# Kernel optimization log

Hardware: AMD Instinct MI355X
Metric: run time of the kernel (lower is better)

The kernel has to match this reference:

```python
import jax, jax.numpy as jnp
import numpy as np

B, F, L = 16384, 32, 64
FEAT, DOM, R = 100000, 8, 16
D_IN = F * L  # 2048
N_HIDDEN = 3  # hidden_units = [256, 128, 1]


def _p(k, shape, scale=0.05):
    return jax.random.normal(k, shape, dtype=jnp.float32) * scale


def setup_inputs() -> dict:
    key = jax.random.key(0)
    ks = jax.random.split(key, 32)
    return {
        'x': jax.random.randint(ks[0], (B, F), 0, FEAT),
        'd': jax.random.randint(ks[1], (B,), 0, DOM),
        'emb': _p(ks[2], (FEAT, L)),
        # share MLP: 2048 -> 1024 -> 512 (ReLU after each)
        'sW0': _p(ks[3], (D_IN, 1024)), 'sb0': _p(ks[4], (1024,)),
        'sW1': _p(ks[5], (1024, 512)), 'sb1': _p(ks[6], (512,)),
        # domain layer: 512 -> 256 shared kernel + per-domain LoRA
        'Dk0': _p(ks[7], (512, 256)), 'Db0': _p(ks[8], (256,)),
        'DA0': _p(ks[9], (DOM, 512, R)), 'DB0': _p(ks[10], (DOM, R, 256)), 'Dlb0': _p(ks[11], (DOM, 256)),
        # task layers: 256 -> 128 -> 1 shared kernels + per-task LoRA
        'Tk0': _p(ks[12], (256, 128)), 'Tb0': _p(ks[13], (128,)),
        'Tk1': _p(ks[14], (128, 1)), 'Tb1': _p(ks[15], (1,)),
        'TA0': _p(ks[16], (2, 256, R)), 'TB0': _p(ks[17], (2, R, 128)), 'Tlb0': _p(ks[18], (2, 128)),
        'TA1': _p(ks[19], (2, 128, R)), 'TB1': _p(ks[20], (2, R, 1)), 'Tlb1': _p(ks[21], (2, 1)),
        # gate hypernet + heads
        'gW0': _p(ks[22], (D_IN, 1024)), 'gb0': _p(ks[23], (1024,)),
        'gW1': _p(ks[24], (1024, 512)), 'gb1': _p(ks[25], (512,)),
        'h0W': _p(ks[26], (512, 4)), 'h0b': _p(ks[27], (4,)),
        'h1W': _p(ks[28], (512, 4)), 'h1b': _p(ks[29], (4,)),
    }


def _mlp2(x, W0, b0, W1, b1):
    return jax.nn.relu(jax.nn.relu(x @ W0 + b0) @ W1 + b1)


def _forward(x, d, emb, sW0, sb0, sW1, sb1, Dk0, Db0, DA0, DB0, Dlb0,
             Tk0, Tb0, Tk1, Tb1, TA0, TB0, Tlb0, TA1, TB1, Tlb1,
             gW0, gb0, gW1, gb1, h0W, h0b, h1W, h1b):
    x_emb = emb[x].reshape(x.shape[0], -1)          # (B, dnn_dim)
    x_dnn = _mlp2(x_emb, sW0, sb0, sW1, sb1)        # (B, 512)

    # ---- domain layer (i=0), k=0 -> ReLU applied ----
    share = x_dnn @ Dk0 + Db0                        # (B, 256)
    lora = jnp.einsum('bi,bir->br', x_dnn, DA0[d])   # per-sample domain LoRA gather+matmul
    lora = jnp.einsum('br,bro->bo', lora, DB0[d]) + Dlb0[d]
    d_dnn = jax.nn.relu(share + lora)                # activated
    # d_share / d_lora kept PRE-activation, as in source

    t_dnn = [d_dnn, d_dnn]
    t_share = [share, share]
    t_lora = [lora, lora]
    t_sl, t_ls = [], []
    Tk, Tb = [Tk0, Tk1], [Tb0, Tb1]
    TA, TB, Tlb = [TA0, TA1], [TB0, TB1], [Tlb0, Tlb1]

    k = 1  # shared counter, faithfully incremented per (i, t) step
    for i in range(2):
        for t in range(2):
            ds = t_dnn[t] @ Tk[i] + Tb[i]
            ss = t_share[t] @ Tk[i] + Tb[i]
            ls = t_lora[t] @ Tk[i] + Tb[i]
            t_ls.append(ls)
            A, Bm, lb = TA[i][t], TB[i][t], Tlb[i][t]
            dl = (t_dnn[t] @ A) @ Bm + lb[None, :]
            sl = (t_share[t] @ A) @ Bm + lb[None, :]
            ll = (t_lora[t] @ A) @ Bm + lb[None, :]
            t_dnn[t] = ds + dl
            t_share[t] = ss
            t_lora[t] = ll
            t_sl.append(sl)
            if k + 1 < N_HIDDEN:  # only fires at (i=0, t=0)
                t_dnn[t] = jax.nn.relu(t_dnn[t])
                t_share[t] = jax.nn.relu(t_share[t])
                t_lora[t] = jax.nn.relu(t_lora[t])
                t_sl[t] = jax.nn.relu(t_sl[t])
                t_ls[t] = jax.nn.relu(t_ls[t])
                k += 1

    # ---- gating (hypernet sees detached embedding) ----
    hyper = _mlp2(jax.lax.stop_gradient(x_emb), gW0, gb0, gW1, gb1)
    gates = [jax.nn.sigmoid(hyper @ h0W + h0b), jax.nn.sigmoid(hyper @ h1W + h1b)]

    outs = []
    for t in range(2):
        g = gates[t]
        # t_dnn/t_share/t_lora are (B,1); t_sl[t]/t_ls[t] are (B,128) from i=0 -> broadcast (B,128)
        outs.append(t_dnn[t] - g[:, 0:1] * t_share[t] - g[:, 1:2] * t_lora[t]
                    - g[:, 2:3] * t_sl[t] - g[:, 3:4] * t_ls[t])
    return jnp.stack(outs)  # (2, B, 128)


def reference(x, d, emb, sW0, sb0, sW1, sb1, Dk0, Db0, DA0, DB0, Dlb0,
              Tk0, Tb0, Tk1, Tb1, TA0, TB0, Tlb0, TA1, TB1, Tlb1,
              gW0, gb0, gW1, gb1, h0W, h0b, h1W, h1b):
    return _forward(x, d, emb, sW0, sb0, sW1, sb1, Dk0, Db0, DA0, DB0, Dlb0,
                    Tk0, Tb0, Tk1, Tb1, TA0, TB0, Tlb0, TA1, TB1, Tlb1,
                    gW0, gb0, gW1, gb1, h0W, h0b, h1W, h1b)
```

## Files before the change

kernel.cpp:

```cpp
#include <hip/hip_runtime.h>
#include <hip/hip_bf16.h>

#define BATCH 16384

typedef __attribute__((ext_vector_type(4))) float f32x4;
typedef __attribute__((ext_vector_type(8))) short bf16x8;

__device__ inline float b2f(unsigned short u) {
    union { unsigned u; float f; } c; c.u = ((unsigned)u) << 16; return c.f;
}
__device__ inline unsigned short f2b(float f) {
    __hip_bfloat16 h = __float2bfloat16(f);
    return *(unsigned short*)&h;
}

#define GLL16(g, l)                                                            \
    __builtin_amdgcn_global_load_lds(                                          \
        (const __attribute__((address_space(1))) void*)(g),                    \
        (__attribute__((address_space(3))) void*)(l), 16, 0, 0)

__global__ __launch_bounds__(256) void k_prep(
    const float* __restrict__ sW0, const float* __restrict__ gW0,
    const float* __restrict__ sW1, const float* __restrict__ gW1,
    const float* __restrict__ Dk0, const float* __restrict__ Tk0,
    const float* __restrict__ TA0,
    const float* __restrict__ sb0, const float* __restrict__ gb0,
    const float* __restrict__ sb1, const float* __restrict__ gb1,
    const float* __restrict__ Tb0, const float* __restrict__ DA0,
    const float* __restrict__ DB0, const float* __restrict__ emb,
    unsigned short* __restrict__ W1t, unsigned short* __restrict__ W2cat,
    unsigned short* __restrict__ Dk0t, unsigned short* __restrict__ Tcat,
    float* __restrict__ b1cat, float* __restrict__ b2cat, float* __restrict__ tb0c,
    unsigned short* __restrict__ DA0b, unsigned short* __restrict__ DB0b,
    unsigned short* __restrict__ embB)
{
    int id = blockIdx.x;
    const int tid = threadIdx.x;
    __shared__ float t[32][33];
    auto tcvt = [&](const float* src, int K, int N, unsigned short* dst,
                    int dst_off, int dst_ld, int bx, int by) {
        int k0 = by * 32, n0 = bx * 32;
        int tx = tid & 31, ty = tid >> 5;
        #pragma unroll
        for (int s = 0; s < 32; s += 8) {
            int k = k0 + ty + s, n = n0 + tx;
            t[ty + s][tx] = (k < K && n < N) ? src[(size_t)k * N + n] : 0.f;
        }
        __syncthreads();
        #pragma unroll
        for (int s = 0; s < 32; s += 8) {
            int n = n0 + ty + s, k = k0 + tx;
            if (n < N && k < K)
                dst[(size_t)(dst_off + n) * dst_ld + k] = f2b(t[tx][ty + s]);
        }
    };
    if (id < 4096) { int z = id >> 11, rem = id & 2047;
        tcvt(z ? gW0 : sW0, 2048, 1024, W1t, z * 1024, 2048, rem & 31, rem >> 5); return; }
    id -= 4096;
    if (id < 1024) { int z = id >> 9, rem = id & 511;
        tcvt(z ? gW1 : sW1, 1024, 512, W2cat, z * 512, 1024, rem & 15, rem >> 4); return; }
    id -= 1024;
    if (id < 128) { tcvt(Dk0, 512, 256, Dk0t, 0, 512, id & 7, id >> 3); return; }
    id -= 128;
    if (id < 32)  { tcvt(Tk0, 256, 128, Tcat, 0, 256, id & 3, id >> 2); return; }
    id -= 32;
    if (id < 16)  { int z = id >> 3;
        tcvt(TA0 + z * 256 * 16, 256, 16, Tcat, 128 + z * 16, 256, 0, id & 7); return; }
    id -= 16;
    if (id < 397) {
        int i = id * 256 + tid;
        if (i < 1024)            { b1cat[i] = sb0[i]; return; }
        if (i < 2048)            { b1cat[i] = gb0[i - 1024]; return; }
        if (i < 2560)            { b2cat[i - 2048] = sb1[i - 2048]; return; }
        if (i < 3072)            { b2cat[i - 2560 + 512] = gb1[i - 2560]; return; }
        if (i < 3200)            { tb0c[i - 3072] = Tb0[i - 3072]; return; }
        if (i < 3232)            { tb0c[i - 3200 + 128] = 0.f; return; }
        i -= 3232;
        if (i < 65536)           { DA0b[i] = f2b(DA0[i]); return; }
        i -= 65536;
        if (i < 32768)           { DB0b[i] = f2b(DB0[i]); return; }
        return;
    }
    id -= 397;
    {
        int e = (id * 256 + tid) * 4;
        if (e < 100000 * 64) {
            float4 v = *(const float4*)(emb + e);
            ushort4 o = { f2b(v.x), f2b(v.y), f2b(v.z), f2b(v.w) };
            *(ushort4*)(embB + e) = o;
        }
    }
}

template<int RELU, int OUTBF16, int GATHER>
__global__ __launch_bounds__(512, 2) void k_gemm256(
    const unsigned short* __restrict__ A, int lda, long Az,
    const unsigned short* __restrict__ Bt, int K, long Bz,
    const float* __restrict__ bias, int biasz,
    void* __restrict__ C, int ldc, long Cz,
    int N, const int* __restrict__ xsrc, const unsigned short* __restrict__ embB)
{
    extern __shared__ char smem_raw[];
    const int NT = K >> 6;
    const int tid  = threadIdx.x;
    const int lane = tid & 63;
    const int w    = tid >> 6;
    const int wr   = w >> 2, wc = w & 3;
    const int frow = lane & 15, kg = lane >> 4;
    const int z = blockIdx.z;
    A    += (size_t)z * Az;
    Bt   += (size_t)z * Bz;
    bias += (size_t)z * biasz;

    const int gx  = gridDim.x;
    const int nwg = gx * gridDim.y;
    const int lin = blockIdx.y * gx + blockIdx.x;
    const int qq  = nwg >> 3;
    const int swz = (lin & 7) * qq + (lin >> 3);
    const int bx = swz % gx, by = swz / gx;
    const int row0 = by * 256, col0 = bx * 256;

    const int lch = (lane & 7) ^ ((lane >> 3) & 7);
    const int isA = (lch < 4);
    const int eoBase = lch * 8;
    int* xbT = (int*)(smem_raw + 131072);
    int rrh[4];
    const unsigned short* gsrc[4];
    #pragma unroll
    for (int h = 0; h < 4; ++h) {
        int rr = h * 64 + w * 8 + (lane >> 3);
        rrh[h] = rr;
        if (isA) gsrc[h] = GATHER ? embB : A + (size_t)(row0 + rr) * lda + lch * 8;
        else     gsrc[h] = Bt + (size_t)min(col0 + rr, N - 1) * K + (lch - 4) * 8;
    }
    const int dBase = w * 1024;

    const int pA = (kg ^ (frow & 7)) * 16;
    const int pB = ((4 + kg) ^ (frow & 7)) * 16;
    int aOff[8], bOff[4];
    #pragma unroll
    for (int m = 0; m < 8; ++m) aOff[m] = (wr * 128 + m * 16 + frow) * 128 + pA;
    #pragma unroll
    for (int n = 0; n < 4; ++n) bOff[n] = (wc * 64 + n * 16 + frow) * 128 + pB;

#define STAGE(t_, ks_, slot_) do {                                              \
        int tc_ = min((int)(t_), NT - 1);                                       \
        int o_ = tc_ * 64 + (ks_) * 32;                                         \
        char* d_ = smem_raw + (slot_) * 65536 + (ks_) * 32768 + dBase;          \
        GLL16(gsrc[0] + o_, d_);                                                \
        GLL16(gsrc[1] + o_, d_ + 8192);                                         \
        GLL16(gsrc[2] + o_, d_ + 16384);                                        \
        GLL16(gsrc[3] + o_, d_ + 24576);                                        \
    } while (0)
#define STAGEX(ix_, tcb_, ks_, slot_) do {                                      \
        char* d_ = smem_raw + (slot_) * 65536 + (ks_) * 32768 + dBase;          \
        _Pragma("unroll")                                                       \
        for (int h_ = 0; h_ < 4; ++h_) {                                        \
            const unsigned short* sa_ = embB + (size_t)(ix_)[h_] * 64           \
                                        + (ks_) * 32 + eoBase;                  \
            const unsigned short* sb2_ = gsrc[h_] + (tcb_) * 64 + (ks_) * 32;   \
            GLL16(isA ? sa_ : sb2_, d_ + h_ * 8192);                            \
        }                                                                       \
    } while (0)
#define READS_B(sb_, ks_)                                                       \
        _Pragma("unroll")                                                       \
        for (int n = 0; n < 4; ++n)                                             \
            bfr[n] = *(const bf16x8*)(smem_raw + (sb_) + (ks_) * 32768 + bOff[n]);
#define READS_A(sb_, ks_, mh_)                                                  \
        _Pragma("unroll")                                                       \
        for (int mi = 0; mi < 4; ++mi)                                          \
            afr[mi] = *(const bf16x8*)(smem_raw + (sb_) + (ks_) * 32768 + aOff[(mh_) * 4 + mi]);
#define MFMA16(mh_) do {                                                        \
        __builtin_amdgcn_s_setprio(1);                                          \
        _Pragma("unroll")                                                       \
        for (int mi = 0; mi < 4; ++mi)                                          \
            _Pragma("unroll")                                                   \
            for (int n = 0; n < 4; ++n)                                         \
                acc[(mh_) * 4 + mi][n] = __builtin_amdgcn_mfma_f32_16x16x32_bf16( \
                    bfr[n], afr[mi], acc[(mh_) * 4 + mi][n], 0, 0, 0);          \
        __builtin_amdgcn_s_setprio(0);                                          \
    } while (0)
#define LGKM0 asm volatile("s_waitcnt lgkmcnt(0)" ::: "memory")
#define VM4   asm volatile("s_waitcnt vmcnt(4)" ::: "memory")
#define BAR   __builtin_amdgcn_s_barrier()

    f32x4 acc[8][4] = {};
    bf16x8 afr[4], bfr[4];
    int ixc[4] = {0, 0, 0, 0};

    if (GATHER) {
        const char* xs = (const char*)(xsrc + row0 * 32);
        #pragma unroll
        for (int r = 0; r < 4; ++r)
            GLL16(xs + r * 8192 + w * 1024 + lane * 16,
                  smem_raw + 65536 + r * 8192 + w * 1024);
        asm volatile("s_waitcnt vmcnt(0)" ::: "memory");
        __builtin_amdgcn_s_barrier();
        const int* xlin = (const int*)(smem_raw + 65536);
        #pragma unroll
        for (int r = 0; r < 4; ++r) {
            int i = (r * 512 + tid) * 4;
            int rr_ = i >> 5, tc_ = i & 31;
            int4 vv = *(const int4*)(xlin + i);
            xbT[(tc_ + 0) * 256 + rr_] = vv.x;
            xbT[(tc_ + 1) * 256 + rr_] = vv.y;
            xbT[(tc_ + 2) * 256 + rr_] = vv.z;
            xbT[(tc_ + 3) * 256 + rr_] = vv.w;
        }
        asm volatile("s_waitcnt lgkmcnt(0)" ::: "memory");
        __builtin_amdgcn_s_barrier();
        int ix0[4];
        #pragma unroll
        for (int h = 0; h < 4; ++h) ix0[h] = xbT[rrh[h]];
        STAGEX(ix0, 0, 0, 0); STAGEX(ix0, 0, 1, 0);
        int t1 = min(1, NT - 1);
        #pragma unroll
        for (int h = 0; h < 4; ++h) ixc[h] = xbT[t1 * 256 + rrh[h]];
    } else {
        STAGE(0, 0, 0); STAGE(0, 1, 0);
    }
    VM4; BAR;

    for (int t = 0; t < NT; ++t) {
        const int slot = t & 1, nslot = slot ^ 1;
        const int sb = slot * 65536;
        const int tcn = min(t + 1, NT - 1);
        int ixn[4];
        READS_B(sb, 0); READS_A(sb, 0, 0);
        if (GATHER) STAGEX(ixc, tcn, 0, nslot); else STAGE(t + 1, 0, nslot);
        if (GATHER) {
            int tc2 = min(t + 2, NT - 1);
            #pragma unroll
            for (int h = 0; h < 4; ++h) ixn[h] = xbT[tc2 * 256 + rrh[h]];
        }
        BAR; LGKM0; MFMA16(0); BAR;
        READS_A(sb, 0, 1);
        VM4;
        BAR; LGKM0; MFMA16(1); BAR;
        READS_B(sb, 1); READS_A(sb, 1, 0);
        if (GATHER) STAGEX(ixc, tcn, 1, nslot); else STAGE(t + 1, 1, nslot);
        BAR; LGKM0; MFMA16(0); BAR;
        READS_A(sb, 1, 1);
        VM4;
        BAR; LGKM0; MFMA16(1); BAR;
        if (GATHER) {
            #pragma unroll
            for (int h = 0; h < 4; ++h) ixc[h] = ixn[h];
        }
    }
#undef STAGE
#undef STAGEX
#undef READS_B
#undef READS_A
#undef MFMA16
#undef LGKM0
#undef VM4
#undef BAR

    #pragma unroll
    for (int m = 0; m < 8; ++m) {
        int row = row0 + wr * 128 + m * 16 + frow;
        #pragma unroll
        for (int n = 0; n < 4; ++n) {
            int col = col0 + wc * 64 + n * 16 + kg * 4;
            float4 bv = *(const float4*)(bias + col);
            float v0 = acc[m][n][0] + bv.x, v1 = acc[m][n][1] + bv.y;
            float v2 = acc[m][n][2] + bv.z, v3 = acc[m][n][3] + bv.w;
            if (RELU) {
                v0 = fmaxf(v0, 0.f); v1 = fmaxf(v1, 0.f);
                v2 = fmaxf(v2, 0.f); v3 = fmaxf(v3, 0.f);
            }
            if (OUTBF16) {
                ushort4 o = { f2b(v0), f2b(v1), f2b(v2), f2b(v3) };
                *(ushort4*)((unsigned short*)C + (size_t)z * Cz + (size_t)row * ldc + col) = o;
            } else {
                float4 o = { v0, v1, v2, v3 };
                *(float4*)((float*)C + (size_t)z * Cz + (size_t)row * ldc + col) = o;
            }
        }
    }
}

template<int RELU, int OUTBF16>
__global__ __launch_bounds__(256) void k_gemm(
    const unsigned short* __restrict__ A, int lda,
    const unsigned short* __restrict__ Bt,
    const float* __restrict__ bias,
    void* __restrict__ C, int ldc,
    int N, int K)
{
    __shared__ __align__(16) unsigned short As[128 * 32];
    __shared__ __align__(16) unsigned short Bs[128 * 32];
    const int tid  = threadIdx.x;
    const int lane = tid & 63;
    const int w    = tid >> 6;
    const int wr   = w >> 1, wc = w & 1;
    const int row0 = blockIdx.y * 128;
    const int col0 = blockIdx.x * 128;
    const int frow = lane & 15;
    const int kg   = lane >> 4;
    const int sw   = kg ^ ((frow >> 1) & 3);

    const int srow = w * 32 + (lane >> 2);
    const int csw  = (lane & 3) ^ ((lane >> 3) & 3);
    const int br0  = min(col0 + srow, N - 1);
    const int br1  = min(col0 + srow + 16, N - 1);

    const unsigned short* a0 = A  + (size_t)(row0 + srow) * lda      + csw * 8;
    const unsigned short* a1 = A  + (size_t)(row0 + srow + 16) * lda + csw * 8;
    const unsigned short* b0 = Bt + (size_t)br0 * K + csw * 8;
    const unsigned short* b1 = Bt + (size_t)br1 * K + csw * 8;
    unsigned short* lA0 = As + (w * 2 + 0) * 512;
    unsigned short* lA1 = As + (w * 2 + 1) * 512;
    unsigned short* lB0 = Bs + (w * 2 + 0) * 512;
    unsigned short* lB1 = Bs + (w * 2 + 1) * 512;

    f32x4 acc[4][4] = {};

    for (int bk = 0; bk < K; bk += 32) {
        __syncthreads();
        GLL16(a0 + bk, lA0);
        GLL16(a1 + bk, lA1);
        GLL16(b0 + bk, lB0);
        GLL16(b1 + bk, lB1);
        __syncthreads();
        bf16x8 af[4], bfr[4];
        #pragma unroll
        for (int m = 0; m < 4; ++m)
            af[m] = *(const bf16x8*)&As[(wr * 64 + m * 16 + frow) * 32 + sw * 8];
        #pragma unroll
        for (int n = 0; n < 4; ++n)
            bfr[n] = *(const bf16x8*)&Bs[(wc * 64 + n * 16 + frow) * 32 + sw * 8];
        #pragma unroll
        for (int m = 0; m < 4; ++m)
            #pragma unroll
            for (int n = 0; n < 4; ++n)
                acc[m][n] = __builtin_amdgcn_mfma_f32_16x16x32_bf16(bfr[n], af[m], acc[m][n], 0, 0, 0);
    }

    #pragma unroll
    for (int m = 0; m < 4; ++m) {
        int row = row0 + wr * 64 + m * 16 + frow;
        #pragma unroll
        for (int n = 0; n < 4; ++n) {
            int col = col0 + wc * 64 + n * 16 + kg * 4;
            if (col >= N) continue;
            float4 bv = *(const float4*)(bias + col);
            float v0 = acc[m][n][0] + bv.x, v1 = acc[m][n][1] + bv.y;
            float v2 = acc[m][n][2] + bv.z, v3 = acc[m][n][3] + bv.w;
            if (RELU) {
                v0 = fmaxf(v0, 0.f); v1 = fmaxf(v1, 0.f);
                v2 = fmaxf(v2, 0.f); v3 = fmaxf(v3, 0.f);
            }
            if (OUTBF16) {
                ushort4 o = { f2b(v0), f2b(v1), f2b(v2), f2b(v3) };
                *(ushort4*)((unsigned short*)C + (size_t)row * ldc + col) = o;
            } else {
                float4 o = { v0, v1, v2, v3 };
                *(float4*)((float*)C + (size_t)row * ldc + col) = o;
            }
        }
    }
}

__global__ __launch_bounds__(256) void k_dlora(
    const unsigned short* __restrict__ Xdnn, const int* __restrict__ d,
    const unsigned short* __restrict__ DA0b, const unsigned short* __restrict__ DB0b,
    const float* __restrict__ Dlb0,
    const unsigned short* __restrict__ SHARE,
    unsigned short* __restrict__ LORA, unsigned short* __restrict__ DDNN)
{
    int w = threadIdx.x >> 6, lane = threadIdx.x & 63;
    int b = blockIdx.x * 4 + w;
    int dom = d[b];
    uint4 raw = *(const uint4*)(Xdnn + (size_t)b * 512 + lane * 8);
    const unsigned short* pr = (const unsigned short*)&raw;
    float xv[8];
    #pragma unroll
    for (int j = 0; j < 8; ++j) xv[j] = b2f(pr[j]);

    const unsigned short* Ap = DA0b + ((size_t)dom * 512 + lane * 8) * 16;
    float v[16];
    #pragma unroll
    for (int r = 0; r < 16; ++r) v[r] = 0.f;
    #pragma unroll
    for (int j = 0; j < 8; ++j) {
        uint4 a0 = *(const uint4*)(Ap + j * 16);
        uint4 a1 = *(const uint4*)(Ap + j * 16 + 8);
        const unsigned short* ap = (const unsigned short*)&a0;
        const unsigned short* aq = (const unsigned short*)&a1;
        float xj = xv[j];
        #pragma unroll
        for (int r = 0; r < 8; ++r) v[r]     += xj * b2f(ap[r]);
        #pragma unroll
        for (int r = 0; r < 8; ++r) v[r + 8] += xj * b2f(aq[r]);
    }
    #pragma unroll
    for (int s = 1; s < 64; s <<= 1) {
        #pragma unroll
        for (int r = 0; r < 16; ++r) v[r] += __shfl_xor(v[r], s, 64);
    }
    const unsigned short* Bp = DB0b + (size_t)dom * 16 * 256;
    const float* lbp = Dlb0 + (size_t)dom * 256;
    #pragma unroll
    for (int c = 0; c < 4; ++c) {
        int o = lane + c * 64;
        float a = lbp[o];
        #pragma unroll
        for (int r = 0; r < 16; ++r) a += v[r] * b2f(Bp[r * 256 + o]);
        float sh = b2f(SHARE[(size_t)b * 256 + o]);
        LORA[(size_t)b * 256 + o] = f2b(a);
        DDNN[(size_t)b * 256 + o] = f2b(fmaxf(sh + a, 0.f));
    }
}

__global__ __launch_bounds__(256) void k_tail(
    const float* __restrict__ Yd, const float* __restrict__ Ys, const float* __restrict__ Yl,
    const unsigned short* __restrict__ Hyper,
    const float* __restrict__ TB0, const float* __restrict__ Tlb0,
    const float* __restrict__ Tk1, const float* __restrict__ Tb1,
    const float* __restrict__ TA1, const float* __restrict__ TB1, const float* __restrict__ Tlb1,
    const float* __restrict__ h0W, const float* __restrict__ h0b,
    const float* __restrict__ h1W, const float* __restrict__ h1b,
    float* __restrict__ out)
{
    __shared__ float sTB0[2][16][128];
    __shared__ float sTlb0[2][128];
    __shared__ float sTk1[128];
    __shared__ float sWeff[2][128];
    __shared__ float sY[4][3][160];
    const int tid = threadIdx.x;

    for (int i = tid; i < 4096; i += 256) ((float*)sTB0)[i] = TB0[i];
    if (tid < 256) ((float*)sTlb0)[tid] = Tlb0[tid];
    if (tid < 128) sTk1[tid] = Tk1[tid];
    {
        int t = tid >> 7, j = tid & 127;
        float a = 0.f;
        #pragma unroll
        for (int r = 0; r < 16; ++r) a += TA1[((size_t)t * 128 + j) * 16 + r] * TB1[t * 16 + r];
        sWeff[t][j] = a;
    }
    const float* Yp[3] = {Yd, Ys, Yl};
    int b0 = blockIdx.x * 4;
    for (int i = tid; i < 4 * 3 * 160; i += 256) {
        int s = i / 480, rem = i % 480, st = rem / 160, idx = rem % 160;
        sY[s][st][idx] = Yp[st][(size_t)(b0 + s) * 160 + idx];
    }
    __syncthreads();

    int w = tid >> 6, lane = tid & 63;
    int b = b0 + w;
    const float* yd = sY[w][0];
    const float* ys = sY[w][1];
    const float* yl = sY[w][2];
    int j0 = lane, j1 = lane + 64;

    uint4 hraw = *(const uint4*)(Hyper + (size_t)b * 512 + lane * 8);
    const unsigned short* hp = (const unsigned short*)&hraw;
    float hv[8];
    #pragma unroll
    for (int j = 0; j < 8; ++j) hv[j] = b2f(hp[j]);

    float red[14];
    #pragma unroll
    for (int k = 0; k < 14; ++k) red[k] = 0.f;
    #pragma unroll
    for (int j = 0; j < 8; ++j) {
        float4 w0 = *(const float4*)(h0W + (size_t)(lane * 8 + j) * 4);
        float4 w1 = *(const float4*)(h1W + (size_t)(lane * 8 + j) * 4);
        red[0] += hv[j] * w0.x; red[1] += hv[j] * w0.y; red[2] += hv[j] * w0.z; red[3] += hv[j] * w0.w;
        red[4] += hv[j] * w1.x; red[5] += hv[j] * w1.y; red[6] += hv[j] * w1.z; red[7] += hv[j] * w1.w;
    }

    float SLv[2][2], LSv[2][2];
    #pragma unroll
    for (int t = 0; t < 2; ++t) {
        float lb0 = sTlb0[t][j0], lb1 = sTlb0[t][j1];
        float dl0 = lb0, dl1 = lb1, sl0 = lb0, sl1 = lb1, ll0 = lb0, ll1 = lb1;
        #pragma unroll
        for (int r = 0; r < 16; ++r) {
            float w0v = sTB0[t][r][j0], w1v = sTB0[t][r][j1];
            float ud = yd[128 + t * 16 + r];
            float us = ys[128 + t * 16 + r];
            float ul = yl[128 + t * 16 + r];
            dl0 += ud * w0v; dl1 += ud * w1v;
            sl0 += us * w0v; sl1 += us * w1v;
            ll0 += ul * w0v; ll1 += ul * w1v;
        }
        float D0 = yd[j0] + dl0, D1 = yd[j1] + dl1;
        float S0 = ys[j0],       S1 = ys[j1];
        float L0 = ll0,          L1 = ll1;
        float sl_0 = sl0, sl_1 = sl1;
        float ls_0 = yl[j0], ls_1 = yl[j1];
        if (t == 0) {
            D0 = fmaxf(D0, 0.f); D1 = fmaxf(D1, 0.f);
            S0 = fmaxf(S0, 0.f); S1 = fmaxf(S1, 0.f);
            L0 = fmaxf(L0, 0.f); L1 = fmaxf(L1, 0.f);
            sl_0 = fmaxf(sl_0, 0.f); sl_1 = fmaxf(sl_1, 0.f);
            ls_0 = fmaxf(ls_0, 0.f); ls_1 = fmaxf(ls_1, 0.f);
        }
        SLv[t][0] = sl_0; SLv[t][1] = sl_1;
        LSv[t][0] = ls_0; LSv[t][1] = ls_1;
        float we0 = sWeff[t][j0], we1 = sWeff[t][j1];
        float tk0 = sTk1[j0],     tk1v = sTk1[j1];
        red[8 + t * 3 + 0] = D0 * (tk0 + we0) + D1 * (tk1v + we1);
        red[8 + t * 3 + 1] = S0 * tk0 + S1 * tk1v;
        red[8 + t * 3 + 2] = L0 * we0 + L1 * we1;
    }

    #pragma unroll
    for (int s = 1; s < 64; s <<= 1) {
        #pragma unroll
        for (int k = 0; k < 14; ++k) red[k] += __shfl_xor(red[k], s, 64);
    }

    float Tb1v = Tb1[0];
    #pragma unroll
    for (int t = 0; t < 2; ++t) {
        float fd = red[8 + t * 3 + 0] + Tb1v + Tlb1[t];
        float fs = red[8 + t * 3 + 1] + Tb1v;
        float fl = red[8 + t * 3 + 2] + Tlb1[t];
        const float* hb = t ? h1b : h0b;
        float g0 = 1.f / (1.f + expf(-(red[t * 4 + 0] + hb[0])));
        float g1 = 1.f / (1.f + expf(-(red[t * 4 + 1] + hb[1])));
        float g2 = 1.f / (1.f + expf(-(red[t * 4 + 2] + hb[2])));
        float g3 = 1.f / (1.f + expf(-(red[t * 4 + 3] + hb[3])));
        float base = fd - g0 * fs - g1 * fl;
        size_t o = (size_t)t * BATCH * 128 + (size_t)b * 128;
        out[o + j0] = base - g2 * SLv[t][0] - g3 * LSv[t][0];
        out[o + j1] = base - g2 * SLv[t][1] - g3 * LSv[t][1];
    }
}

extern "C" void kernel_launch(void* const* d_in, const int* in_sizes, int n_in,
                              void* d_out, int out_size, void* d_ws, size_t ws_size,
                              hipStream_t stream)
{
    const int*   x    = (const int*)  d_in[0];
    const int*   dix  = (const int*)  d_in[1];
    const float* emb  = (const float*)d_in[2];
    const float* sW0  = (const float*)d_in[3];
    const float* sb0  = (const float*)d_in[4];
    const float* sW1  = (const float*)d_in[5];
    const float* sb1  = (const float*)d_in[6];
    const float* Dk0  = (const float*)d_in[7];
    const float* Db0  = (const float*)d_in[8];
    const float* DA0  = (const float*)d_in[9];
    const float* DB0  = (const float*)d_in[10];
    const float* Dlb0 = (const float*)d_in[11];
    const float* Tk0  = (const float*)d_in[12];
    const float* Tb0  = (const float*)d_in[13];
    const float* Tk1  = (const float*)d_in[14];
    const float* Tb1  = (const float*)d_in[15];
    const float* TA0  = (const float*)d_in[16];
    const float* TB0  = (const float*)d_in[17];
    const float* Tlb0 = (const float*)d_in[18];
    const float* TA1  = (const float*)d_in[19];
    const float* TB1  = (const float*)d_in[20];
    const float* Tlb1 = (const float*)d_in[21];
    const float* gW0  = (const float*)d_in[22];
    const float* gb0  = (const float*)d_in[23];
    const float* gW1  = (const float*)d_in[24];
    const float* gb1  = (const float*)d_in[25];
    const float* h0W  = (const float*)d_in[26];
    const float* h0b  = (const float*)d_in[27];
    const float* h1W  = (const float*)d_in[28];
    const float* h1b  = (const float*)d_in[29];

    hipFuncSetAttribute((const void*)k_gemm256<1, 1, 1>,
                        hipFuncAttributeMaxDynamicSharedMemorySize, 163840);
    hipFuncSetAttribute((const void*)k_gemm256<1, 1, 0>,
                        hipFuncAttributeMaxDynamicSharedMemorySize, 131072);

    char* ws = (char*)d_ws;
    size_t off = 0;
    auto alloc = [&](size_t bytes) -> void* {
        void* p = ws + off;
        off += (bytes + 255) & ~(size_t)255;
        return p;
    };
    unsigned short* W1t   = (unsigned short*)alloc((size_t)2048 * 2048 * 2);
    unsigned short* W2cat = (unsigned short*)alloc((size_t)1024 * 1024 * 2);
    unsigned short* Dk0t  = (unsigned short*)alloc((size_t)256 * 512 * 2);
    unsigned short* Tcat  = (unsigned short*)alloc((size_t)160 * 256 * 2);
    unsigned short* DA0b  = (unsigned short*)alloc((size_t)8 * 512 * 16 * 2);
    unsigned short* DB0b  = (unsigned short*)alloc((size_t)8 * 16 * 256 * 2);
    unsigned short* embB  = (unsigned short*)alloc((size_t)100000 * 64 * 2);
    float*          b1cat = (float*)alloc(2048 * 4);
    float*          b2cat = (float*)alloc(1024 * 4);
    float*          tb0c  = (float*)alloc(160 * 4);
    float*          Ybase = (float*)alloc((size_t)3 * BATCH * 160 * 4);
    char* regB = (char*)alloc((size_t)BATCH * 2048 * 2);
    unsigned short* Xdnn  = (unsigned short*)alloc((size_t)BATCH * 512 * 2);
    unsigned short* Hyper = (unsigned short*)alloc((size_t)BATCH * 512 * 2);

    float* Ys = Ybase;
    float* Yl = Ybase + (size_t)BATCH * 160;
    float* Yd = Ybase + (size_t)2 * BATCH * 160;
    unsigned short* Hbuf  = (unsigned short*)regB;
    unsigned short* SHARE = (unsigned short*)regB;
    unsigned short* LORA  = SHARE + (size_t)BATCH * 256;
    unsigned short* DDNN  = LORA  + (size_t)BATCH * 256;

    k_prep<<<11943, 256, 0, stream>>>(
        sW0, gW0, sW1, gW1, Dk0, Tk0, TA0,
        sb0, gb0, sb1, gb1, Tb0, DA0, DB0, emb,
        W1t, W2cat, Dk0t, Tcat, b1cat, b2cat, tb0c, DA0b, DB0b, embB);

    k_gemm256<1, 1, 1><<<dim3(8, 64, 1), 512, 163840, stream>>>(
        embB, 0, 0, W1t, 2048, 0, b1cat, 0, Hbuf, 2048, 0, 2048, x, embB);
    k_gemm256<1, 1, 0><<<dim3(2, 64, 2), 512, 131072, stream>>>(
        Hbuf, 2048, 1024, W2cat, 1024, (long)512 * 1024, b2cat, 512,
        Xdnn, 512, (long)BATCH * 512, 512, nullptr, nullptr);
    k_gemm<0, 1><<<dim3(2, 128), 256, 0, stream>>>(Xdnn, 512, Dk0t, Db0, SHARE, 256, 256, 512);
    k_dlora<<<BATCH / 4, 256, 0, stream>>>(Xdnn, dix, DA0b, DB0b, Dlb0, SHARE, LORA, DDNN);
    k_gemm<0, 0><<<dim3(2, 384), 256, 0, stream>>>(SHARE, 256, Tcat, tb0c, Ybase, 160, 160, 256);
    k_tail<<<BATCH / 4, 256, 0, stream>>>(Yd, Ys, Yl, Hyper, TB0, Tlb0, Tk1, Tb1,
                                          TA1, TB1, Tlb1, h0W, h0b, h1W, h1b, (float*)d_out);
}
```

Before: 350.8 us.

## Merge GEMM main-loop phases into two full-K steps with fewer barriers

The GEMM main loop now loads all eight A fragments and four B fragments per k-half and issues 32 MFMAs at once, replacing the four half-phases that each had a barrier before and after. That cuts the per-tile barrier count from eight to two and drops the explicit lgkmcnt waits, letting the compiler schedule the LDS reads against the MFMAs. The transposed index buffer xbT is also XOR-swizzled to avoid LDS bank conflicts when the gather indices are written. The cost is more fragment registers and looser wave synchronisation, which could reduce occupancy or let waves contend on the next slot's staging.

```diff
diff --git a/kernel.cpp b/kernel.cpp
--- a/kernel.cpp
+++ b/kernel.cpp
@@ -162,30 +162,29 @@
             GLL16(isA ? sa_ : sb2_, d_ + h_ * 8192);                            \
         }                                                                       \
     } while (0)
-#define READS_B(sb_, ks_)                                                       \
+#define READS(sb_, ks_) do {                                                    \
         _Pragma("unroll")                                                       \
         for (int n = 0; n < 4; ++n)                                             \
-            bfr[n] = *(const bf16x8*)(smem_raw + (sb_) + (ks_) * 32768 + bOff[n]);
-#define READS_A(sb_, ks_, mh_)                                                  \
+            bfr[n] = *(const bf16x8*)(smem_raw + (sb_) + (ks_) * 32768 + bOff[n]); \
         _Pragma("unroll")                                                       \
-        for (int mi = 0; mi < 4; ++mi)                                          \
-            afr[mi] = *(const bf16x8*)(smem_raw + (sb_) + (ks_) * 32768 + aOff[(mh_) * 4 + mi]);
-#define MFMA16(mh_) do {                                                        \
+        for (int mi = 0; mi < 8; ++mi)                                          \
+            afr[mi] = *(const bf16x8*)(smem_raw + (sb_) + (ks_) * 32768 + aOff[mi]); \
+    } while (0)
+#define MFMA32() do {                                                           \
         __builtin_amdgcn_s_setprio(1);                                          \
         _Pragma("unroll")                                                       \
-        for (int mi = 0; mi < 4; ++mi)                                          \
+        for (int mi = 0; mi < 8; ++mi)                                          \
             _Pragma("unroll")                                                   \
             for (int n = 0; n < 4; ++n)                                         \
-                acc[(mh_) * 4 + mi][n] = __builtin_amdgcn_mfma_f32_16x16x32_bf16( \
-                    bfr[n], afr[mi], acc[(mh_) * 4 + mi][n], 0, 0, 0);          \
+                acc[mi][n] = __builtin_amdgcn_mfma_f32_16x16x32_bf16(           \
+                    bfr[n], afr[mi], acc[mi][n], 0, 0, 0);                      \
         __builtin_amdgcn_s_setprio(0);                                          \
     } while (0)
-#define LGKM0 asm volatile("s_waitcnt lgkmcnt(0)" ::: "memory")
 #define VM4   asm volatile("s_waitcnt vmcnt(4)" ::: "memory")
-#define BAR   __builtin_amdgcn_s_barrier()
+#define BARM  asm volatile("s_barrier" ::: "memory")
 
     f32x4 acc[8][4] = {};
-    bf16x8 afr[4], bfr[4];
+    bf16x8 afr[8], bfr[4];
     int ixc[4] = {0, 0, 0, 0};
 
     if (GATHER) {
@@ -195,54 +194,50 @@
             GLL16(xs + r * 8192 + w * 1024 + lane * 16,
                   smem_raw + 65536 + r * 8192 + w * 1024);
         asm volatile("s_waitcnt vmcnt(0)" ::: "memory");
-        __builtin_amdgcn_s_barrier();
+        BARM;
         const int* xlin = (const int*)(smem_raw + 65536);
         #pragma unroll
         for (int r = 0; r < 4; ++r) {
             int i = (r * 512 + tid) * 4;
             int rr_ = i >> 5, tc_ = i & 31;
             int4 vv = *(const int4*)(xlin + i);
-            xbT[(tc_ + 0) * 256 + rr_] = vv.x;
-            xbT[(tc_ + 1) * 256 + rr_] = vv.y;
-            xbT[(tc_ + 2) * 256 + rr_] = vv.z;
-            xbT[(tc_ + 3) * 256 + rr_] = vv.w;
+            xbT[(tc_ + 0) * 256 + (rr_ ^ ((tc_ + 0) & 31))] = vv.x;
+            xbT[(tc_ + 1) * 256 + (rr_ ^ ((tc_ + 1) & 31))] = vv.y;
+            xbT[(tc_ + 2) * 256 + (rr_ ^ ((tc_ + 2) & 31))] = vv.z;
+            xbT[(tc_ + 3) * 256 + (rr_ ^ ((tc_ + 3) & 31))] = vv.w;
         }
         asm volatile("s_waitcnt lgkmcnt(0)" ::: "memory");
-        __builtin_amdgcn_s_barrier();
+        BARM;
         int ix0[4];
         #pragma unroll
         for (int h = 0; h < 4; ++h) ix0[h] = xbT[rrh[h]];
         STAGEX(ix0, 0, 0, 0); STAGEX(ix0, 0, 1, 0);
         int t1 = min(1, NT - 1);
         #pragma unroll
-        for (int h = 0; h < 4; ++h) ixc[h] = xbT[t1 * 256 + rrh[h]];
+        for (int h = 0; h < 4; ++h) ixc[h] = xbT[t1 * 256 + (rrh[h] ^ (t1 & 31))];
     } else {
         STAGE(0, 0, 0); STAGE(0, 1, 0);
     }
-    VM4; BAR;
+    VM4; BARM;
 
     for (int t = 0; t < NT; ++t) {
         const int slot = t & 1, nslot = slot ^ 1;
         const int sb = slot * 65536;
         const int tcn = min(t + 1, NT - 1);
         int ixn[4];
-        READS_B(sb, 0); READS_A(sb, 0, 0);
+        READS(sb, 0);
         if (GATHER) STAGEX(ixc, tcn, 0, nslot); else STAGE(t + 1, 0, nslot);
         if (GATHER) {
             int tc2 = min(t + 2, NT - 1);
             #pragma unroll
-            for (int h = 0; h < 4; ++h) ixn[h] = xbT[tc2 * 256 + rrh[h]];
-        }
-        BAR; LGKM0; MFMA16(0); BAR;
-        READS_A(sb, 0, 1);
-        VM4;
-        BAR; LGKM0; MFMA16(1); BAR;
-        READS_B(sb, 1); READS_A(sb, 1, 0);
+            for (int h = 0; h < 4; ++h) ixn[h] = xbT[tc2 * 256 + (rrh[h] ^ (tc2 & 31))];
+        }
+        MFMA32();
+        VM4; BARM;
+        READS(sb, 1);
         if (GATHER) STAGEX(ixc, tcn, 1, nslot); else STAGE(t + 1, 1, nslot);
-        BAR; LGKM0; MFMA16(0); BAR;
-        READS_A(sb, 1, 1);
-        VM4;
-        BAR; LGKM0; MFMA16(1); BAR;
+        MFMA32();
+        VM4; BARM;
         if (GATHER) {
             #pragma unroll
             for (int h = 0; h < 4; ++h) ixc[h] = ixn[h];
@@ -250,12 +245,10 @@
     }
 #undef STAGE
 #undef STAGEX
-#undef READS_B
-#undef READS_A
-#undef MFMA16
-#undef LGKM0
+#undef READS
+#undef MFMA32
 #undef VM4
-#undef BAR
+#undef BARM
 
     #pragma unroll
     for (int m = 0; m < 8; ++m) {
```

Result: no change. 344.7 us (-1.7%).
